# Kernel optimization log

Hardware: AMD Instinct MI355X
Metric: run time of the kernel (lower is better)

## Reference

```python
import jax, jax.numpy as jnp
import numpy as np

N_NODES = 50000
N_EDGES = 600000
DIM_IN = 128
DIM_OUT = 128


def setup_inputs() -> dict:
    key = jax.random.key(0)
    k1, k2, k3, k4, k5 = jax.random.split(key, 5)
    x = jax.random.normal(k1, (N_NODES, DIM_IN), dtype=jnp.float32)
    # torch Linear weight is [dim_out, dim_in]
    W = jax.random.normal(k2, (DIM_OUT, DIM_IN), dtype=jnp.float32) * (1.0 / np.sqrt(DIM_IN))
    vals = jax.random.uniform(k3, (N_EDGES,), dtype=jnp.float32)
    rows = jax.random.randint(k4, (N_EDGES,), 0, N_NODES, dtype=jnp.int64)
    cols = jax.random.randint(k5, (N_EDGES,), 0, N_NODES, dtype=jnp.int64)
    return {"x": x, "W": W, "vals": vals, "rows": rows, "cols": cols}


def reference(x, W, vals, rows, cols):
    # Linear (no bias): h = x @ W^T, shape [N, dim_out]
    h = x @ W.T
    # Sparse adjacency SpMM in COO form: out[i] = sum_{e: rows[e]==i} vals[e] * h[cols[e]]
    msg = vals[:, None] * h[cols]  # [E, dim_out]
    out = jax.ops.segment_sum(msg, rows, num_segments=x.shape[0])
    return jax.nn.relu(out)
```

## Files before the change

kernel.cpp:

```cpp
#include <hip/hip_runtime.h>

#define N_NODES 50000
#define N_EDGES 600000
#define DIM 128
#define NB 782
#define EPB 768
#define GCAP 2048

typedef short bf16x8 __attribute__((ext_vector_type(8)));
typedef float f32x4 __attribute__((ext_vector_type(4)));

__device__ __forceinline__ float bf2f(unsigned short u) {
    union { unsigned int i; float f; } x; x.i = ((unsigned int)u) << 16; return x.f;
}
__device__ __forceinline__ unsigned short f2bf(float f) {
    union { float f; unsigned int i; } x; x.f = f;
    unsigned int r = x.i + 0x7FFFu + ((x.i >> 16) & 1u);
    return (unsigned short)(r >> 16);
}

#define GEMM_BLOCKS NB

__global__ __launch_bounds__(256) void gemm_kernel(const float* __restrict__ x,
                                                   const float* __restrict__ W,
                                                   unsigned short* __restrict__ h,
                                                   const int* __restrict__ rows,
                                                   int* __restrict__ Hm) {
    __shared__ unsigned char Wl[128 * 256];
    __shared__ int cntL[NB];
    const int tid = threadIdx.x;

    if (Hm) {
        for (int i = tid; i < NB; i += 256) cntL[i] = 0;
    }

#pragma unroll
    for (int i = 0; i < 16; ++i) {
        int c  = tid + i * 256;
        int od = c >> 5;
        int kg = c & 31;
        float4 w = *((const float4*)(W + od * DIM) + kg);
        unsigned int lo = (unsigned int)f2bf(w.x) | ((unsigned int)f2bf(w.y) << 16);
        unsigned int hi = (unsigned int)f2bf(w.z) | ((unsigned int)f2bf(w.w) << 16);
        int byte = od * 256 + ((kg * 8) ^ ((od & 7) << 4));
        *reinterpret_cast<uint2*>(Wl + byte) = make_uint2(lo, hi);
    }

    const int lane = tid & 63;
    const int wv   = tid >> 6;
    const int q    = lane >> 4;
    const int node = blockIdx.x * 64 + wv * 16 + (lane & 15);
    const int ncl  = node < N_NODES ? node : N_NODES - 1;

    bf16x8 xb[4];
#pragma unroll
    for (int s = 0; s < 4; ++s) {
        const float* xp = x + (size_t)ncl * DIM + s * 32 + q * 8;
        float4 x0 = *(const float4*)(xp);
        float4 x1 = *(const float4*)(xp + 4);
        bf16x8 v;
        v[0] = (short)f2bf(x0.x); v[1] = (short)f2bf(x0.y);
        v[2] = (short)f2bf(x0.z); v[3] = (short)f2bf(x0.w);
        v[4] = (short)f2bf(x1.x); v[5] = (short)f2bf(x1.y);
        v[6] = (short)f2bf(x1.z); v[7] = (short)f2bf(x1.w);
        xb[s] = v;
    }

    __syncthreads();

    if (Hm) {
        int ebase = blockIdx.x * EPB;
#pragma unroll
        for (int i = 0; i < 3; ++i) {
            int e = ebase + tid + i * 256;
            if (e < N_EDGES) atomicAdd(&cntL[rows[e] >> 6], 1);
        }
    }

#pragma unroll
    for (int dt = 0; dt < 8; ++dt) {
        f32x4 acc = {0.f, 0.f, 0.f, 0.f};
        const int od = dt * 16 + (lane & 15);
#pragma unroll
        for (int s = 0; s < 4; ++s) {
            int byte = od * 256 + ((s * 64 + q * 16) ^ ((od & 7) << 4));
            bf16x8 a = *reinterpret_cast<const bf16x8*>(Wl + byte);
            acc = __builtin_amdgcn_mfma_f32_16x16x32_bf16(a, xb[s], acc, 0, 0, 0);
        }
        if (node < N_NODES) {
            unsigned int lo = (unsigned int)f2bf(acc[0]) | ((unsigned int)f2bf(acc[1]) << 16);
            unsigned int hi = (unsigned int)f2bf(acc[2]) | ((unsigned int)f2bf(acc[3]) << 16);
            *reinterpret_cast<uint2*>(h + (size_t)node * DIM + dt * 16 + q * 4) = make_uint2(lo, hi);
        }
    }

    if (Hm) {
        __syncthreads();
        int* Hrow = Hm + (size_t)blockIdx.x * NB;
        for (int i = tid; i < NB; i += 256) Hrow[i] = cntL[i];
    }
}

__global__ __launch_bounds__(256) void scanA_kernel(int* __restrict__ Hm,
                                                    int* __restrict__ tot) {
    int gw   = (blockIdx.x * 256 + threadIdx.x) >> 6;
    int lane = threadIdx.x & 63;
    if (gw >= NB) return;
    int carry = 0;
    for (int ch = 0; ch < 13; ++ch) {
        int j = ch * 64 + lane;
        int v = (j < NB) ? Hm[(size_t)j * NB + gw] : 0;
        int incl = v;
#pragma unroll
        for (int d = 1; d < 64; d <<= 1) {
            int t = __shfl_up(incl, d);
            if (lane >= d) incl += t;
        }
        if (j < NB) Hm[(size_t)j * NB + gw] = carry + incl - v;
        carry += __shfl(incl, 63);
    }
    if (lane == 0) tot[gw] = carry;
}

__global__ __launch_bounds__(1024) void scanB_kernel(const int* __restrict__ tot,
                                                     int* __restrict__ boff) {
    __shared__ int s[1024];
    int t = threadIdx.x;
    int v = (t < NB) ? tot[t] : 0;
    s[t] = v;
    __syncthreads();
    for (int d = 1; d < 1024; d <<= 1) {
        int a = (t >= d) ? s[t - d] : 0;
        __syncthreads();
        s[t] += a;
        __syncthreads();
    }
    if (t < NB) boff[t] = s[t] - v;
    if (t == 0) boff[NB] = N_EDGES;
}

__global__ __launch_bounds__(256) void scatter_kernel(const int* __restrict__ rows,
                                                      const int* __restrict__ cols,
                                                      const float* __restrict__ vals,
                                                      const int* __restrict__ Hm,
                                                      const int* __restrict__ boff,
                                                      int2* __restrict__ erec) {
    __shared__ int cl[NB];
    int tid = threadIdx.x, j = blockIdx.x;
    const int* Hrow = Hm + (size_t)j * NB;
    for (int i = tid; i < NB; i += 256) cl[i] = boff[i] + Hrow[i];
    __syncthreads();
    int ebase = j * EPB;
#pragma unroll
    for (int i = 0; i < 3; ++i) {
        int e = ebase + tid + i * 256;
        if (e < N_EDGES) {
            int r = rows[e];
            int slot = atomicAdd(&cl[r >> 6], 1);
            int2 rec;
            rec.x = cols[e] | ((r & 63) << 16);
            rec.y = __float_as_int(vals[e]);
            erec[slot] = rec;
        }
    }
}

__global__ __launch_bounds__(256) void gather_kernel(const unsigned short* __restrict__ h,
                                                     const int2* __restrict__ erec,
                                                     const int* __restrict__ boff,
                                                     float* __restrict__ out) {
    __shared__ int2 srt[GCAP];
    __shared__ int hist[64];
    __shared__ int cursor[64];
    __shared__ int starts[65];
    int tid = threadIdx.x, b = blockIdx.x;
    int beg = boff[b], end = boff[b + 1];
    int cnt = end - beg;
    int w = tid >> 6, lane = tid & 63;

    if (tid < 64) hist[tid] = 0;
    __syncthreads();

    if (cnt <= GCAP) {
        int2 rec[8];
        int  rr[8];
#pragma unroll
        for (int k = 0; k < 8; ++k) {
            int i = tid + k * 256;
            if (i < cnt) {
                rec[k] = erec[beg + i];
                rr[k] = (rec[k].x >> 16) & 63;
                atomicAdd(&hist[rr[k]], 1);
            }
        }
        __syncthreads();
        if (tid < 64) {
            int v = hist[tid], incl = v;
#pragma unroll
            for (int d = 1; d < 64; d <<= 1) {
                int t = __shfl_up(incl, d);
                if (tid >= d) incl += t;
            }
            starts[tid] = incl - v;
            cursor[tid] = incl - v;
            if (tid == 63) starts[64] = incl;
        }
        __syncthreads();
#pragma unroll
        for (int k = 0; k < 8; ++k) {
            int i = tid + k * 256;
            if (i < cnt) {
                int pos = atomicAdd(&cursor[rr[k]], 1);
                srt[pos] = rec[k];
            }
        }
        __syncthreads();
        for (int t0 = 0; t0 < 16; ++t0) {
            int t = w * 16 + t0;
            int node = b * 64 + t;
            int s0 = starts[t], s1 = starts[t + 1];
            float ax = 0.f, ay = 0.f;
            int i = s0;
            for (; i + 4 <= s1; i += 4) {
                int2 r0 = srt[i], r1 = srt[i + 1], r2 = srt[i + 2], r3 = srt[i + 3];
                ushort2 a0 = *((const ushort2*)(h + (size_t)(r0.x & 0xFFFF) * DIM) + lane);
                ushort2 a1 = *((const ushort2*)(h + (size_t)(r1.x & 0xFFFF) * DIM) + lane);
                ushort2 a2 = *((const ushort2*)(h + (size_t)(r2.x & 0xFFFF) * DIM) + lane);
                ushort2 a3 = *((const ushort2*)(h + (size_t)(r3.x & 0xFFFF) * DIM) + lane);
                float v0 = __int_as_float(r0.y), v1 = __int_as_float(r1.y);
                float v2 = __int_as_float(r2.y), v3 = __int_as_float(r3.y);
                ax += v0 * bf2f(a0.x) + v1 * bf2f(a1.x) + v2 * bf2f(a2.x) + v3 * bf2f(a3.x);
                ay += v0 * bf2f(a0.y) + v1 * bf2f(a1.y) + v2 * bf2f(a2.y) + v3 * bf2f(a3.y);
            }
            for (; i < s1; ++i) {
                int2 r0 = srt[i];
                ushort2 a0 = *((const ushort2*)(h + (size_t)(r0.x & 0xFFFF) * DIM) + lane);
                float v0 = __int_as_float(r0.y);
                ax += v0 * bf2f(a0.x);
                ay += v0 * bf2f(a0.y);
            }
            if (node < N_NODES) {
                float2 o;
                o.x = fmaxf(ax, 0.f);
                o.y = fmaxf(ay, 0.f);
                *reinterpret_cast<float2*>(&out[(size_t)node * DIM + lane * 2]) = o;
            }
        }
    } else {
        for (int t0 = 0; t0 < 16; ++t0) {
            int t = w * 16 + t0;
            int node = b * 64 + t;
            float ax = 0.f, ay = 0.f;
            for (int i = 0; i < cnt; ++i) {
                int2 r = erec[beg + i];
                if (((r.x >> 16) & 63) == t) {
                    ushort2 a = *((const ushort2*)(h + (size_t)(r.x & 0xFFFF) * DIM) + lane);
                    float v = __int_as_float(r.y);
                    ax += v * bf2f(a.x);
                    ay += v * bf2f(a.y);
                }
            }
            if (node < N_NODES) {
                float2 o;
                o.x = fmaxf(ax, 0.f);
                o.y = fmaxf(ay, 0.f);
                *reinterpret_cast<float2*>(&out[(size_t)node * DIM + lane * 2]) = o;
            }
        }
    }
}

__global__ __launch_bounds__(256) void edge_kernel(const unsigned short* __restrict__ h,
                                                   const float* __restrict__ vals,
                                                   const int* __restrict__ rows,
                                                   const int* __restrict__ cols,
                                                   float* __restrict__ out) {
    long long gid = (long long)blockIdx.x * 256 + threadIdx.x;
    int e    = (int)(gid >> 5);
    int lane = (int)(gid & 31);
    if (e >= N_EDGES) return;
    int r = rows[e];
    int c = cols[e];
    float v = vals[e];
    ushort4 hv = *((const ushort4*)(h + (size_t)c * DIM) + lane);
    float* op = &out[(size_t)r * DIM + lane * 4];
    atomicAdd(op + 0, v * bf2f(hv.x));
    atomicAdd(op + 1, v * bf2f(hv.y));
    atomicAdd(op + 2, v * bf2f(hv.z));
    atomicAdd(op + 3, v * bf2f(hv.w));
}

__global__ __launch_bounds__(256) void relu_kernel(float* __restrict__ out) {
    int i = blockIdx.x * 256 + threadIdx.x;
    float4* p = reinterpret_cast<float4*>(out) + i;
    float4 v = *p;
    v.x = fmaxf(v.x, 0.f);
    v.y = fmaxf(v.y, 0.f);
    v.z = fmaxf(v.z, 0.f);
    v.w = fmaxf(v.w, 0.f);
    *p = v;
}

extern "C" void kernel_launch(void* const* d_in, const int* in_sizes, int n_in,
                              void* d_out, int out_size, void* d_ws, size_t ws_size,
                              hipStream_t stream) {
    const float* x    = (const float*)d_in[0];
    const float* W    = (const float*)d_in[1];
    const float* vals = (const float*)d_in[2];
    const int*   rows = (const int*)d_in[3];
    const int*   cols = (const int*)d_in[4];
    float* out = (float*)d_out;

    unsigned short* h = (unsigned short*)d_ws;
    int2* erec = (int2*)(h + (size_t)N_NODES * DIM);
    int*  Hm   = (int*)(erec + N_EDGES);
    int*  tot  = Hm + (size_t)NB * NB;
    int*  boff = tot + NB;
    size_t need = (size_t)((char*)(boff + NB + 1) - (char*)d_ws);

    if (ws_size >= need) {
        gemm_kernel<<<GEMM_BLOCKS, 256, 0, stream>>>(x, W, h, rows, Hm);
        scanA_kernel<<<(NB * 64 + 255) / 256, 256, 0, stream>>>(Hm, tot);
        scanB_kernel<<<1, 1024, 0, stream>>>(tot, boff);
        scatter_kernel<<<NB, 256, 0, stream>>>(rows, cols, vals, Hm, boff, erec);
        gather_kernel<<<NB, 256, 0, stream>>>(h, erec, boff, out);
    } else {
        gemm_kernel<<<GEMM_BLOCKS, 256, 0, stream>>>(x, W, h, nullptr, nullptr);
        hipMemsetAsync(d_out, 0, (size_t)N_NODES * DIM * sizeof(float), stream);
        edge_kernel<<<(N_EDGES * 32) / 256, 256, 0, stream>>>(h, vals, rows, cols, out);
        relu_kernel<<<(N_NODES * DIM / 4) / 256, 256, 0, stream>>>(out);
    }
}
```

Before: 80.75 us.

## Split each gather row across half-waves with 8-byte loads and 512-thread blocks

Result: faster. 68.79 us (-14.8%).

```diff
diff --git a/kernel.cpp b/kernel.cpp
--- a/kernel.cpp
+++ b/kernel.cpp
@@ -165,7 +165,7 @@
     }
 }
 
-__global__ __launch_bounds__(256) void gather_kernel(const unsigned short* __restrict__ h,
+__global__ __launch_bounds__(512) void gather_kernel(const unsigned short* __restrict__ h,
                                                      const int2* __restrict__ erec,
                                                      const int* __restrict__ boff,
                                                      float* __restrict__ out) {
@@ -177,16 +177,18 @@
     int beg = boff[b], end = boff[b + 1];
     int cnt = end - beg;
     int w = tid >> 6, lane = tid & 63;
+    int pos = lane & 31;
+    int half = lane >> 5;
 
     if (tid < 64) hist[tid] = 0;
     __syncthreads();
 
     if (cnt <= GCAP) {
-        int2 rec[8];
-        int  rr[8];
-#pragma unroll
-        for (int k = 0; k < 8; ++k) {
-            int i = tid + k * 256;
+        int2 rec[4];
+        int  rr[4];
+#pragma unroll
+        for (int k = 0; k < 4; ++k) {
+            int i = tid + k * 512;
             if (i < cnt) {
                 rec[k] = erec[beg + i];
                 rr[k] = (rec[k].x >> 16) & 63;
@@ -207,64 +209,82 @@
         }
         __syncthreads();
 #pragma unroll
-        for (int k = 0; k < 8; ++k) {
-            int i = tid + k * 256;
+        for (int k = 0; k < 4; ++k) {
+            int i = tid + k * 512;
             if (i < cnt) {
-                int pos = atomicAdd(&cursor[rr[k]], 1);
-                srt[pos] = rec[k];
-            }
-        }
-        __syncthreads();
-        for (int t0 = 0; t0 < 16; ++t0) {
-            int t = w * 16 + t0;
+                int pos2 = atomicAdd(&cursor[rr[k]], 1);
+                srt[pos2] = rec[k];
+            }
+        }
+        __syncthreads();
+        for (int t0 = 0; t0 < 8; ++t0) {
+            int t = w * 8 + t0;
             int node = b * 64 + t;
             int s0 = starts[t], s1 = starts[t + 1];
-            float ax = 0.f, ay = 0.f;
-            int i = s0;
-            for (; i + 4 <= s1; i += 4) {
-                int2 r0 = srt[i], r1 = srt[i + 1], r2 = srt[i + 2], r3 = srt[i + 3];
-                ushort2 a0 = *((const ushort2*)(h + (size_t)(r0.x & 0xFFFF) * DIM) + lane);
-                ushort2 a1 = *((const ushort2*)(h + (size_t)(r1.x & 0xFFFF) * DIM) + lane);
-                ushort2 a2 = *((const ushort2*)(h + (size_t)(r2.x & 0xFFFF) * DIM) + lane);
-                ushort2 a3 = *((const ushort2*)(h + (size_t)(r3.x & 0xFFFF) * DIM) + lane);
+            float a0 = 0.f, a1 = 0.f, a2 = 0.f, a3 = 0.f;
+            int i = s0 + half;
+            for (; i + 6 < s1; i += 8) {
+                int2 r0 = srt[i], r1 = srt[i + 2], r2 = srt[i + 4], r3 = srt[i + 6];
+                ushort4 h0 = *((const ushort4*)(h + (size_t)(r0.x & 0xFFFF) * DIM) + pos);
+                ushort4 h1 = *((const ushort4*)(h + (size_t)(r1.x & 0xFFFF) * DIM) + pos);
+                ushort4 h2 = *((const ushort4*)(h + (size_t)(r2.x & 0xFFFF) * DIM) + pos);
+                ushort4 h3 = *((const ushort4*)(h + (size_t)(r3.x & 0xFFFF) * DIM) + pos);
                 float v0 = __int_as_float(r0.y), v1 = __int_as_float(r1.y);
                 float v2 = __int_as_float(r2.y), v3 = __int_as_float(r3.y);
-                ax += v0 * bf2f(a0.x) + v1 * bf2f(a1.x) + v2 * bf2f(a2.x) + v3 * bf2f(a3.x);
-                ay += v0 * bf2f(a0.y) + v1 * bf2f(a1.y) + v2 * bf2f(a2.y) + v3 * bf2f(a3.y);
-            }
-            for (; i < s1; ++i) {
+                a0 += v0 * bf2f(h0.x) + v1 * bf2f(h1.x) + v2 * bf2f(h2.x) + v3 * bf2f(h3.x);
+                a1 += v0 * bf2f(h0.y) + v1 * bf2f(h1.y) + v2 * bf2f(h2.y) + v3 * bf2f(h3.y);
+                a2 += v0 * bf2f(h0.z) + v1 * bf2f(h1.z) + v2 * bf2f(h2.z) + v3 * bf2f(h3.z);
+                a3 += v0 * bf2f(h0.w) + v1 * bf2f(h1.w) + v2 * bf2f(h2.w) + v3 * bf2f(h3.w);
+            }
+            for (; i < s1; i += 2) {
                 int2 r0 = srt[i];
-                ushort2 a0 = *((const ushort2*)(h + (size_t)(r0.x & 0xFFFF) * DIM) + lane);
+                ushort4 h0 = *((const ushort4*)(h + (size_t)(r0.x & 0xFFFF) * DIM) + pos);
                 float v0 = __int_as_float(r0.y);
-                ax += v0 * bf2f(a0.x);
-                ay += v0 * bf2f(a0.y);
-            }
-            if (node < N_NODES) {
-                float2 o;
-                o.x = fmaxf(ax, 0.f);
-                o.y = fmaxf(ay, 0.f);
-                *reinterpret_cast<float2*>(&out[(size_t)node * DIM + lane * 2]) = o;
+                a0 += v0 * bf2f(h0.x);
+                a1 += v0 * bf2f(h0.y);
+                a2 += v0 * bf2f(h0.z);
+                a3 += v0 * bf2f(h0.w);
+            }
+            a0 += __shfl_xor(a0, 32);
+            a1 += __shfl_xor(a1, 32);
+            a2 += __shfl_xor(a2, 32);
+            a3 += __shfl_xor(a3, 32);
+            if (half == 0 && node < N_NODES) {
+                float4 o;
+                o.x = fmaxf(a0, 0.f);
+                o.y = fmaxf(a1, 0.f);
+                o.z = fmaxf(a2, 0.f);
+                o.w = fmaxf(a3, 0.f);
+                *reinterpret_cast<float4*>(&out[(size_t)node * DIM + pos * 4]) = o;
             }
         }
     } else {
-        for (int t0 = 0; t0 < 16; ++t0) {
-            int t = w * 16 + t0;
+        for (int t0 = 0; t0 < 8; ++t0) {
+            int t = w * 8 + t0;
             int node = b * 64 + t;
-            float ax = 0.f, ay = 0.f;
-            for (int i = 0; i < cnt; ++i) {
+            float a0 = 0.f, a1 = 0.f, a2 = 0.f, a3 = 0.f;
+            for (int i = half; i < cnt; i += 2) {
                 int2 r = erec[beg + i];
                 if (((r.x >> 16) & 63) == t) {
-                    ushort2 a = *((const ushort2*)(h + (size_t)(r.x & 0xFFFF) * DIM) + lane);
+                    ushort4 hv = *((const ushort4*)(h + (size_t)(r.x & 0xFFFF) * DIM) + pos);
                     float v = __int_as_float(r.y);
-                    ax += v * bf2f(a.x);
-                    ay += v * bf2f(a.y);
+                    a0 += v * bf2f(hv.x);
+                    a1 += v * bf2f(hv.y);
+                    a2 += v * bf2f(hv.z);
+                    a3 += v * bf2f(hv.w);
                 }
             }
-            if (node < N_NODES) {
-                float2 o;
-                o.x = fmaxf(ax, 0.f);
-                o.y = fmaxf(ay, 0.f);
-                *reinterpret_cast<float2*>(&out[(size_t)node * DIM + lane * 2]) = o;
+            a0 += __shfl_xor(a0, 32);
+            a1 += __shfl_xor(a1, 32);
+            a2 += __shfl_xor(a2, 32);
+            a3 += __shfl_xor(a3, 32);
+            if (half == 0 && node < N_NODES) {
+                float4 o;
+                o.x = fmaxf(a0, 0.f);
+                o.y = fmaxf(a1, 0.f);
+                o.z = fmaxf(a2, 0.f);
+                o.w = fmaxf(a3, 0.f);
+                *reinterpret_cast<float4*>(&out[(size_t)node * DIM + pos * 4]) = o;
             }
         }
     }
@@ -323,7 +343,7 @@
         scanA_kernel<<<(NB * 64 + 255) / 256, 256, 0, stream>>>(Hm, tot);
         scanB_kernel<<<1, 1024, 0, stream>>>(tot, boff);
         scatter_kernel<<<NB, 256, 0, stream>>>(rows, cols, vals, Hm, boff, erec);
-        gather_kernel<<<NB, 256, 0, stream>>>(h, erec, boff, out);
+        gather_kernel<<<NB, 512, 0, stream>>>(h, erec, boff, out);
     } else {
         gemm_kernel<<<GEMM_BLOCKS, 256, 0, stream>>>(x, W, h, nullptr, nullptr);
         hipMemsetAsync(d_out, 0, (size_t)N_NODES * DIM * sizeof(float), stream);
```
